# Optimization experiments

Measured on AMD Instinct MI355X. Metric: run time of the kernel, lower is better.

The kernel has to match this reference:

```python
import jax, jax.numpy as jnp
import numpy as np

IN_FEATURES = 4096
OUT_FEATURES = 4096
BATCH = 8192


def setup_inputs() -> dict:
    key = jax.random.key(0)
    k1, k2 = jax.random.split(key)
    x = jax.random.normal(k1, (BATCH, IN_FEATURES), dtype=jnp.float32)
    # nn.init.normal_(vals, std=1/sqrt(in_features))
    vals = jax.random.normal(k2, (IN_FEATURES + OUT_FEATURES - 1,), dtype=jnp.float32) / np.sqrt(IN_FEATURES)
    return {"x": x, "vals": vals}


def _build_weight(vals):
    # W[i, j] = vals[(out_features - 1 - i) + j]  -> constant diagonals (Toeplitz)
    idx = jnp.arange(IN_FEATURES)                      # [in]
    row_offsets = jnp.arange(OUT_FEATURES - 1, -1, -1)  # [out], descending
    indices = row_offsets[:, None] + idx[None, :]       # [out, in]
    return vals[indices]


def reference(x, vals):
    W = _build_weight(vals)          # [out, in]
    return x @ W.T                   # [B, out]
```

## Files before the change

### kernel.cpp

```cpp
#include <hip/hip_runtime.h>
#include <stdint.h>

#define MM 8192
#define NN 4096
#define KK 4096
#define BM 256
#define BN 256
#define BK 64
#define NT (KK / BK)

typedef __attribute__((ext_vector_type(8))) short short8;
typedef __attribute__((ext_vector_type(4))) float floatx4;
typedef int int4a __attribute__((ext_vector_type(4), aligned(4)));

__device__ inline unsigned short f2bf(float f) {
    unsigned int u = __float_as_uint(f);
    u += 0x7FFFu + ((u >> 16) & 1u);
    return (unsigned short)(u >> 16);
}

__global__ void prep_x_kernel(const float* __restrict__ x, unsigned short* __restrict__ xb) {
    size_t i = (size_t)blockIdx.x * 256 + threadIdx.x;
    const float4* x4 = (const float4*)x;
    float4 v0 = x4[i * 2];
    float4 v1 = x4[i * 2 + 1];
    ushort4 o0, o1;
    o0.x = f2bf(v0.x); o0.y = f2bf(v0.y); o0.z = f2bf(v0.z); o0.w = f2bf(v0.w);
    o1.x = f2bf(v1.x); o1.y = f2bf(v1.y); o1.z = f2bf(v1.z); o1.w = f2bf(v1.w);
    *(ushort4*)(xb + i * 8)     = o0;
    *(ushort4*)(xb + i * 8 + 4) = o1;
}

__global__ void prep_vals_kernel(const float* __restrict__ vals,
                                 unsigned short* __restrict__ vlo,
                                 unsigned short* __restrict__ vhi) {
    int i = blockIdx.x * 256 + threadIdx.x;
    if (i < KK + NN - 1) {
        unsigned short s = f2bf(vals[i]);
        vlo[i] = s;
        if (i > 0) vhi[i - 1] = s;
    }
}

#define GLOAD_LDS16(g, l)                                              \
    __builtin_amdgcn_global_load_lds(                                  \
        (__attribute__((address_space(1))) void*)(g),                  \
        (__attribute__((address_space(3))) void*)(l), 16, 0, 0)

__global__ __launch_bounds__(512, 2) void gemm_kernel(
        const unsigned short* __restrict__ A,
        const unsigned short* __restrict__ vlo,
        const unsigned short* __restrict__ vhi,
        float* __restrict__ C) {
    __shared__ unsigned short ldsA[4][BM * BK];

    const int tid  = threadIdx.x;
    const int lane = tid & 63;
    const int w    = tid >> 6;
    const int n0 = blockIdx.x * BN;
    const int m0 = blockIdx.y * BM;

    const int quad = lane >> 4;
    const int l16  = lane & 15;
    const int wm   = (w >> 2) * 128;
    const int wn   = (w & 3) * 64;

    const int lr8 = lane >> 3;
    const int cg  = (lane & 7) ^ (lr8 & 7);
    const unsigned short* aSrc = A + (size_t)(m0 + w * 32 + lr8) * KK + cg * 8;
    const int sBase = (w * 32) * BK;

    const unsigned short* bptr[4];
#pragma unroll
    for (int j = 0; j < 4; ++j) {
        int idx0 = (NN - 1) - (n0 + wn + l16) - j * 16 + quad * 8;
        bptr[j] = (idx0 & 1) ? (vhi + (idx0 - 1)) : (vlo + idx0);
    }

    floatx4 acc[8][4] = {};
    short8 b0r[8], b1r[8];
    short8 afA[4], afB[4];

#define STAGE1(BI, T, G)                                               \
    GLOAD_LDS16(aSrc + (size_t)(G) * 8 * KK + (size_t)(T) * BK,        \
                &ldsA[BI][sBase + (G) * 8 * BK])

#define LOADB(DST, T)                                                  \
    do {                                                               \
        _Pragma("unroll")                                              \
        for (int j = 0; j < 4; ++j) {                                  \
            _Pragma("unroll")                                          \
            for (int kh = 0; kh < 2; ++kh) {                           \
                int4a t_ = *(const int4a*)(bptr[j] + (size_t)(T) * BK + kh * 32); \
                __builtin_memcpy(&(DST)[j * 2 + kh], &t_, 16);         \
            }                                                          \
        }                                                              \
    } while (0)

#define AFRAG(AF, BI, P)                                               \
    do {                                                               \
        _Pragma("unroll")                                              \
        for (int ii = 0; ii < 2; ++ii) {                               \
            _Pragma("unroll")                                          \
            for (int kh = 0; kh < 2; ++kh)                             \
                (AF)[ii * 2 + kh] = *(const short8*)&ldsA[BI][         \
                    (wm + (2 * (P) + ii) * 16 + l16) * BK +            \
                    (((kh * 4 + quad) ^ (l16 & 7)) * 8)];              \
        }                                                              \
    } while (0)

#define MFMA16(AF, BS, P)                                              \
    do {                                                               \
        _Pragma("unroll")                                              \
        for (int kh = 0; kh < 2; ++kh) {                               \
            _Pragma("unroll")                                          \
            for (int ii = 0; ii < 2; ++ii) {                           \
                _Pragma("unroll")                                      \
                for (int j = 0; j < 4; ++j)                            \
                    acc[2 * (P) + ii][j] =                             \
                        __builtin_amdgcn_mfma_f32_16x16x32_bf16(       \
                            (AF)[ii * 2 + kh], (BS)[j * 2 + kh],       \
                            acc[2 * (P) + ii][j], 0, 0, 0);            \
            }                                                          \
        }                                                              \
    } while (0)

#define SB()                                                           \
    do {                                                               \
        asm volatile("" ::: "memory");                                 \
        __builtin_amdgcn_s_barrier();                                  \
        asm volatile("" ::: "memory");                                 \
    } while (0)
#define PRIO(x) __builtin_amdgcn_s_setprio(x)
#define WAITV(N) asm volatile("s_waitcnt vmcnt(" #N ")" ::: "memory")

#pragma unroll
    for (int g = 0; g < 4; ++g) STAGE1(0, 0, g);
    LOADB(b0r, 0);
#pragma unroll
    for (int g = 0; g < 4; ++g) STAGE1(1, 1, g);
    WAITV(12);
    SB();
    AFRAG(afA, 0, 0);

#define TILE(BI, T, BCUR, BNXT, DOB, DOST, DONXT, LW)                  \
    do {                                                               \
        if (DOB) LOADB(BNXT, (T) + 1);                                 \
        AFRAG(afB, BI, 1);                                             \
        if (DOST) STAGE1(((BI) + 2) & 3, (T) + 2, 0);                  \
        PRIO(1); MFMA16(afA, BCUR, 0); PRIO(0);                        \
        AFRAG(afA, BI, 2);                                             \
        if (DOST) STAGE1(((BI) + 2) & 3, (T) + 2, 1);                  \
        PRIO(1); MFMA16(afB, BCUR, 1); PRIO(0);                        \
        AFRAG(afB, BI, 3);                                             \
        if (DOST) STAGE1(((BI) + 2) & 3, (T) + 2, 2);                  \
        PRIO(1); MFMA16(afA, BCUR, 2); PRIO(0);                        \
        if (DOST) STAGE1(((BI) + 2) & 3, (T) + 2, 3);                  \
        LW;                                                            \
        if (DONXT) { SB(); AFRAG(afA, ((BI) + 1) & 3, 0); }            \
        PRIO(1); MFMA16(afB, BCUR, 3); PRIO(0);                        \
    } while (0)

    for (int u = 0; u < 15; ++u) {
        const int t = u * 4;
        TILE(0, t + 0, b0r, b1r, 1, 1, 1, WAITV(12));
        TILE(1, t + 1, b1r, b0r, 1, 1, 1, WAITV(12));
        TILE(2, t + 2, b0r, b1r, 1, 1, 1, WAITV(12));
        TILE(3, t + 3, b1r, b0r, 1, 1, 1, WAITV(12));
    }
    TILE(0, 60, b0r, b1r, 1, 1, 1, WAITV(12));
    TILE(1, 61, b1r, b0r, 1, 1, 1, WAITV(12));
    TILE(2, 62, b0r, b1r, 1, 0, 1, WAITV(8));
    TILE(3, 63, b1r, b0r, 0, 0, 0, (void)0);

    float* cW = C + (size_t)(m0 + wm) * NN + (n0 + wn);
#pragma unroll
    for (int i = 0; i < 8; ++i) {
#pragma unroll
        for (int j = 0; j < 4; ++j) {
            float* cp = cW + (size_t)(i * 16 + quad * 4) * NN + j * 16 + l16;
#pragma unroll
            for (int r = 0; r < 4; ++r)
                cp[(size_t)r * NN] = acc[i][j][r];
        }
    }
#undef TILE
#undef STAGE1
#undef LOADB
#undef AFRAG
#undef MFMA16
}

extern "C" void kernel_launch(void* const* d_in, const int* in_sizes, int n_in,
                              void* d_out, int out_size, void* d_ws, size_t ws_size,
                              hipStream_t stream) {
    const float* x    = (const float*)d_in[0];
    const float* vals = (const float*)d_in[1];
    float* out = (float*)d_out;

    unsigned short* xb  = (unsigned short*)d_ws;
    unsigned short* vlo = xb + (size_t)MM * KK;
    unsigned short* vhi = vlo + 16384;

    prep_x_kernel<<<MM * KK / 8 / 256, 256, 0, stream>>>(x, xb);
    prep_vals_kernel<<<(KK + NN - 1 + 255) / 256, 256, 0, stream>>>(vals, vlo, vhi);

    dim3 grid(NN / BN, MM / BM);
    gemm_kernel<<<grid, 512, 0, stream>>>(xb, vlo, vhi, out);
}
```

Measured before the change: 453.7 us.

## Stage Toeplitz diagonal window into LDS and use triple-buffered A tiles

Each block now copies the slice of the bf16 diagonal vector it needs into LDS once, stored as four shifted copies so every alignment offset can be read with 8-byte LDS loads. Per-tile B fragments then come from LDS instead of global memory. To make room, the A staging ring drops from four buffers to three, with the tile rotation and vmcnt waits changed to match. The aim is to cut repeated global/L2 traffic for B, at the cost of a shallower A prefetch pipeline, extra LDS reads and possible bank conflicts.

```diff
diff --git a/kernel.cpp b/kernel.cpp
--- a/kernel.cpp
+++ b/kernel.cpp
@@ -7,7 +7,8 @@
 #define BM 256
 #define BN 256
 #define BK 64
-#define NT (KK / BK)
+
+#define BW_STRIDE 4376
 
 typedef __attribute__((ext_vector_type(8))) short short8;
 typedef __attribute__((ext_vector_type(4))) float floatx4;
@@ -52,7 +53,8 @@
         const unsigned short* __restrict__ vlo,
         const unsigned short* __restrict__ vhi,
         float* __restrict__ C) {
-    __shared__ unsigned short ldsA[4][BM * BK];
+    __shared__ unsigned short ldsA[3][BM * BK];
+    __shared__ unsigned short ldsB[4 * BW_STRIDE];
 
     const int tid  = threadIdx.x;
     const int lane = tid & 63;
@@ -70,11 +72,13 @@
     const unsigned short* aSrc = A + (size_t)(m0 + w * 32 + lr8) * KK + cg * 8;
     const int sBase = (w * 32) * BK;
 
-    const unsigned short* bptr[4];
+    const int w0 = (NN - 1) - 255 - n0;
+    const unsigned short* bp[4];
 #pragma unroll
     for (int j = 0; j < 4; ++j) {
         int idx0 = (NN - 1) - (n0 + wn + l16) - j * 16 + quad * 8;
-        bptr[j] = (idx0 & 1) ? (vhi + (idx0 - 1)) : (vlo + idx0);
+        int s = idx0 & 3;
+        bp[j] = ldsB + s * BW_STRIDE + (idx0 - s - w0);
     }
 
     floatx4 acc[8][4] = {};
@@ -91,8 +95,13 @@
         for (int j = 0; j < 4; ++j) {                                  \
             _Pragma("unroll")                                          \
             for (int kh = 0; kh < 2; ++kh) {                           \
-                int4a t_ = *(const int4a*)(bptr[j] + (size_t)(T) * BK + kh * 32); \
-                __builtin_memcpy(&(DST)[j * 2 + kh], &t_, 16);         \
+                const unsigned short* p_ = bp[j] + (T) * BK + kh * 32; \
+                uint2 lo_ = *(const uint2*)p_;                         \
+                uint2 hi_ = *(const uint2*)(p_ + 4);                   \
+                short8 f_;                                             \
+                __builtin_memcpy(&f_, &lo_, 8);                        \
+                __builtin_memcpy((char*)&f_ + 8, &hi_, 8);             \
+                (DST)[j * 2 + kh] = f_;                                \
             }                                                          \
         }                                                              \
     } while (0)
@@ -134,44 +143,63 @@
 #define PRIO(x) __builtin_amdgcn_s_setprio(x)
 #define WAITV(N) asm volatile("s_waitcnt vmcnt(" #N ")" ::: "memory")
 
+    {
+        const unsigned short* bsrc0 = vlo + w0;
+        const unsigned short* bsrc1 = vhi + w0;
+        const unsigned short* bsrc2 = vlo + w0 + 2;
+        const unsigned short* bsrc3 = vhi + w0 + 2;
+#pragma unroll
+        for (int s = 0; s < 4; ++s) {
+            const unsigned short* sp = (s == 0) ? bsrc0 : (s == 1) ? bsrc1
+                                     : (s == 2) ? bsrc2 : bsrc3;
+            unsigned short* dp = ldsB + s * BW_STRIDE;
+            int4a v = *(const int4a*)(sp + (size_t)tid * 8);
+            *(int4a*)(dp + tid * 8) = v;
+            if (tid < 32) {
+                int4a v2 = *(const int4a*)(sp + (size_t)(512 + tid) * 8);
+                *(int4a*)(dp + (512 + tid) * 8) = v2;
+            }
+        }
+    }
 #pragma unroll
     for (int g = 0; g < 4; ++g) STAGE1(0, 0, g);
+#pragma unroll
+    for (int g = 0; g < 4; ++g) STAGE1(1, 1, g);
+    __syncthreads();
     LOADB(b0r, 0);
-#pragma unroll
-    for (int g = 0; g < 4; ++g) STAGE1(1, 1, g);
-    WAITV(12);
-    SB();
     AFRAG(afA, 0, 0);
 
-#define TILE(BI, T, BCUR, BNXT, DOB, DOST, DONXT, LW)                  \
+#define TILE(BI, BIN, BI2, T, BCUR, BNXT, DOB, DOST, DONXT, LW)        \
     do {                                                               \
         if (DOB) LOADB(BNXT, (T) + 1);                                 \
         AFRAG(afB, BI, 1);                                             \
-        if (DOST) STAGE1(((BI) + 2) & 3, (T) + 2, 0);                  \
+        if (DOST) STAGE1(BI2, (T) + 2, 0);                             \
         PRIO(1); MFMA16(afA, BCUR, 0); PRIO(0);                        \
         AFRAG(afA, BI, 2);                                             \
-        if (DOST) STAGE1(((BI) + 2) & 3, (T) + 2, 1);                  \
+        if (DOST) STAGE1(BI2, (T) + 2, 1);                             \
         PRIO(1); MFMA16(afB, BCUR, 1); PRIO(0);                        \
         AFRAG(afB, BI, 3);                                             \
-        if (DOST) STAGE1(((BI) + 2) & 3, (T) + 2, 2);                  \
+        if (DOST) STAGE1(BI2, (T) + 2, 2);                             \
         PRIO(1); MFMA16(afA, BCUR, 2); PRIO(0);                        \
-        if (DOST) STAGE1(((BI) + 2) & 3, (T) + 2, 3);                  \
+        if (DOST) STAGE1(BI2, (T) + 2, 3);                             \
         LW;                                                            \
-        if (DONXT) { SB(); AFRAG(afA, ((BI) + 1) & 3, 0); }            \
+        if (DONXT) { SB(); AFRAG(afA, BIN, 0); }                       \
         PRIO(1); MFMA16(afB, BCUR, 3); PRIO(0);                        \
     } while (0)
 
-    for (int u = 0; u < 15; ++u) {
-        const int t = u * 4;
-        TILE(0, t + 0, b0r, b1r, 1, 1, 1, WAITV(12));
-        TILE(1, t + 1, b1r, b0r, 1, 1, 1, WAITV(12));
-        TILE(2, t + 2, b0r, b1r, 1, 1, 1, WAITV(12));
-        TILE(3, t + 3, b1r, b0r, 1, 1, 1, WAITV(12));
-    }
-    TILE(0, 60, b0r, b1r, 1, 1, 1, WAITV(12));
-    TILE(1, 61, b1r, b0r, 1, 1, 1, WAITV(12));
-    TILE(2, 62, b0r, b1r, 1, 0, 1, WAITV(8));
-    TILE(3, 63, b1r, b0r, 0, 0, 0, (void)0);
+    for (int v = 0; v < 10; ++v) {
+        const int t = v * 6;
+        TILE(0, 1, 2, t + 0, b0r, b1r, 1, 1, 1, WAITV(4));
+        TILE(1, 2, 0, t + 1, b1r, b0r, 1, 1, 1, WAITV(4));
+        TILE(2, 0, 1, t + 2, b0r, b1r, 1, 1, 1, WAITV(4));
+        TILE(0, 1, 2, t + 3, b1r, b0r, 1, 1, 1, WAITV(4));
+        TILE(1, 2, 0, t + 4, b0r, b1r, 1, 1, 1, WAITV(4));
+        TILE(2, 0, 1, t + 5, b1r, b0r, 1, 1, 1, WAITV(4));
+    }
+    TILE(0, 1, 2, 60, b0r, b1r, 1, 1, 1, WAITV(4));
+    TILE(1, 2, 0, 61, b1r, b0r, 1, 1, 1, WAITV(4));
+    TILE(2, 0, 1, 62, b0r, b1r, 1, 0, 1, WAITV(0));
+    TILE(0, 1, 2, 63, b1r, b0r, 0, 0, 0, (void)0);
 
     float* cW = C + (size_t)(m0 + wm) * NN + (n0 + wn);
 #pragma unroll
```

New measurement: 432.9 us. 4.6% less time.
